# Performance work log

Hardware: AMD Instinct MI355X
Metric: run time of the kernel (lower is better)

Reference implementation:

```python
import jax, jax.numpy as jnp
import numpy as np

D_MODEL = 1024
N_HEADS = 16
N_GROUPS = 4
D_K = D_MODEL // N_HEADS
HEADS_PER_GROUP = N_HEADS // N_GROUPS


def rope(x):
    # x: [b, s, d]; rotate using half-split concat (NOT interleaved), matching source
    s, d = x.shape[1], x.shape[2]
    theta = 1.0 / (10000.0 ** (jnp.arange(d // 2, dtype=jnp.float32) / (d // 2)))
    ang = jnp.arange(s, dtype=jnp.float32)[:, None] * theta[None, :]  # [s, d/2]
    cos, sin = jnp.cos(ang), jnp.sin(ang)
    xe, xo = x[..., 0::2], x[..., 1::2]
    return jnp.concatenate([xe * cos - xo * sin, xe * sin + xo * cos], axis=-1)


def setup_inputs() -> dict:
    key = jax.random.key(0)
    k1, k2, k3, k4, k5 = jax.random.split(key, 5)
    b, s = 1, 2048
    scale = 0.02
    X = jax.random.normal(k1, (b, s, D_MODEL), dtype=jnp.float32)
    W_q = jax.random.normal(k2, (D_MODEL, D_MODEL), dtype=jnp.float32) * scale
    W_k = jax.random.normal(k3, (N_GROUPS * D_K, D_MODEL), dtype=jnp.float32) * scale
    W_v = jax.random.normal(k4, (N_GROUPS * D_K, D_MODEL), dtype=jnp.float32) * scale
    W_o = jax.random.normal(k5, (D_MODEL, D_MODEL), dtype=jnp.float32) * scale
    return {"X": X, "W_q": W_q, "W_k": W_k, "W_v": W_v, "W_o": W_o}


def reference(X, W_q, W_k, W_v, W_o):
    b, s, _ = X.shape
    Xr = rope(X)
    Q = (Xr @ W_q.T).reshape(b, s, N_HEADS, D_K).transpose(0, 2, 1, 3)
    K = (Xr @ W_k.T).reshape(b, s, N_GROUPS, D_K).transpose(0, 2, 1, 3)
    V = (Xr @ W_v.T).reshape(b, s, N_GROUPS, D_K).transpose(0, 2, 1, 3)
    Q = Q.reshape(b, N_GROUPS, HEADS_PER_GROUP, s, D_K)
    scores = jnp.einsum('bghsd,bgtd->bghst', Q, K) / jnp.sqrt(jnp.float32(D_K))
    mask = jnp.triu(jnp.ones((s, s), dtype=scores.dtype), k=1) * (-1e9)
    attn = jax.nn.softmax(scores + mask, axis=-1)
    out = jnp.einsum('bghst,bgtd->bghsd', attn, V)  # [b,g,h,s,dk]
    out = out.reshape(b, N_HEADS, s, D_K).transpose(0, 2, 1, 3).reshape(b, s, D_MODEL)
    return out @ W_o.T
```

## Files before the change

kernel.cpp:

```cpp
#include <hip/hip_runtime.h>
#include <hip/hip_bf16.h>

#define S_LEN   2048
#define D_MODEL 1024
#define N_HEADS 16
#define N_GROUPS 4
#define D_K     64
#define KV_DIM  (N_GROUPS * D_K)

typedef __hip_bfloat16 bf16;
typedef unsigned short u16;
typedef __attribute__((ext_vector_type(8))) short bfrag;
typedef __attribute__((ext_vector_type(4))) float ffrag;
typedef __attribute__((ext_vector_type(4))) unsigned int u32x4;

__device__ __forceinline__ float b2f(u16 u) {
    return __uint_as_float(((unsigned)u) << 16);
}
__device__ __forceinline__ u16 f2bu(float f) {
    bf16 h = __float2bfloat16(f);
    return __builtin_bit_cast(u16, h);
}
__device__ __forceinline__ unsigned cvt_pk_bf16(float lo, float hi) {
    unsigned r;
    asm("v_cvt_pk_bf16_f32 %0, %1, %2" : "=v"(r) : "v"(lo), "v"(hi));
    return r;
}
__device__ __forceinline__ float max3f(float a, float b, float c) {
    float d;
    asm("v_max3_f32 %0, %1, %2, %3" : "=v"(d) : "v"(a), "v"(b), "v"(c));
    return d;
}
__device__ __forceinline__ float ex2(float x) {
#if __has_builtin(__builtin_amdgcn_exp2f)
    return __builtin_amdgcn_exp2f(x);
#else
    return __expf(x * 0.69314718f);
#endif
}

typedef __attribute__((address_space(3))) u16 lds_u16;
typedef __attribute__((address_space(1))) const u16 glb_u16;
__device__ __forceinline__ void gld_lds16(const u16* g, u16* l) {
    __builtin_amdgcn_global_load_lds((glb_u16*)g, (lds_u16*)l, 16, 0, 0);
}

__device__ __forceinline__ int posCS3(int i, int c) {
    if (i >= 4 * c + 3)
        return (c == 0) ? i - 3 : (c == 1) ? i + 6 : (c == 2) ? i + 11 : 27;
    int dd = i - 4 * c + 1;
    return 28 + (3 - dd) * 4 + c;
}

__device__ __forceinline__ int probe_f32(const u16* p) {
    int lane = threadIdx.x & 63;
    int e0 = (p[lane] >> 7) & 0xFF;
    int e1 = (p[lane + 64] >> 7) & 0xFF;
    int c = ((e0 < 100 || e0 > 140) ? 1 : 0) + ((e1 < 100 || e1 > 140) ? 1 : 0);
    unsigned long long b1 = __ballot(c >= 1);
    unsigned long long b2 = __ballot(c >= 2);
    return ((__popcll(b1) + __popcll(b2)) > 16) ? 1 : 0;
}

__global__ void probe5_kernel(const u16* __restrict__ p0, const u16* __restrict__ p1,
                              const u16* __restrict__ p2, const u16* __restrict__ p3,
                              const u16* __restrict__ p4, int* __restrict__ mode) {
    if (blockIdx.x != 0) return;
    const u16* ps[5] = {p0, p1, p2, p3, p4};
    int lane = threadIdx.x & 63;
    for (int t = 0; t < 5; t++) {
        int e0 = (ps[t][lane] >> 7) & 0xFF;
        int e1 = (ps[t][lane + 64] >> 7) & 0xFF;
        int c = ((e0 < 100 || e0 > 140) ? 1 : 0) + ((e1 < 100 || e1 > 140) ? 1 : 0);
        unsigned long long b1 = __ballot(c >= 1);
        unsigned long long b2 = __ballot(c >= 2);
        if (lane == 0) mode[t] = ((__popcll(b1) + __popcll(b2)) > 16) ? 1 : 0;
    }
}

__global__ __launch_bounds__(512)
void prep_kernel(const void* __restrict__ Xin, u16* __restrict__ Xr,
                 const void* __restrict__ Wq, const void* __restrict__ Wk,
                 const void* __restrict__ Wv, const void* __restrict__ Wo,
                 u16* __restrict__ WB, u16* __restrict__ WoB) {
    int b = blockIdx.x;
    if (b < S_LEN) {
        int md = probe_f32((const u16*)Xin);
        int i = b;
        int j = threadIdx.x;
        float freq = ex2(-(float)j * 0.025952563241307518f);
        float ang  = (float)i * freq;
        float sv, cv;
        sincosf(ang, &sv, &cv);
        int base = i * D_MODEL;
        float xe, xo;
        if (md) {
            float2 xv = *(const float2*)&((const float*)Xin)[base + 2 * j];
            xe = xv.x; xo = xv.y;
        } else {
            ushort2 xv = *(const ushort2*)&((const u16*)Xin)[base + 2 * j];
            xe = b2f(xv.x); xo = b2f(xv.y);
        }
        Xr[base + j]       = f2bu(xe * cv - xo * sv);
        Xr[base + 512 + j] = f2bu(xe * sv + xo * cv);
    } else {
        int bid = b - S_LEN;
        const void* src; u16* dst; int goff;
        if (bid < 256)      { src = Wq; dst = WB;               goff = bid; }
        else if (bid < 320) { src = Wk; dst = WB + 1024 * 1024; goff = bid - 256; }
        else if (bid < 384) { src = Wv; dst = WB + 1280 * 1024; goff = bid - 320; }
        else                { src = Wo; dst = WoB;              goff = bid - 384; }
        int md = probe_f32((const u16*)src);
        size_t g = (size_t)goff * 512 + threadIdx.x;
        if (md) {
            const float* f = (const float*)src + g * 8;
            float4 v0 = *(const float4*)f;
            float4 v1 = *(const float4*)(f + 4);
            u16 t[8] = {f2bu(v0.x), f2bu(v0.y), f2bu(v0.z), f2bu(v0.w),
                        f2bu(v1.x), f2bu(v1.y), f2bu(v1.z), f2bu(v1.w)};
            *(uint4*)(dst + g * 8) = *(const uint4*)t;
        } else {
            *(uint4*)(dst + g * 8) = *(const uint4*)((const u16*)src + g * 8);
        }
    }
}

__global__ __launch_bounds__(512)
void rope_kernel(const void* __restrict__ Xin, u16* __restrict__ Xr) {
    int md = probe_f32((const u16*)Xin);
    int i = blockIdx.x;
    int j = threadIdx.x;
    float freq = ex2(-(float)j * 0.025952563241307518f);
    float ang  = (float)i * freq;
    float sv, cv;
    sincosf(ang, &sv, &cv);
    int base = i * D_MODEL;
    float xe, xo;
    if (md) {
        float2 xv = *(const float2*)&((const float*)Xin)[base + 2 * j];
        xe = xv.x; xo = xv.y;
    } else {
        ushort2 xv = *(const ushort2*)&((const u16*)Xin)[base + 2 * j];
        xe = b2f(xv.x); xo = b2f(xv.y);
    }
    Xr[base + j]       = f2bu(xe * cv - xo * sv);
    Xr[base + 512 + j] = f2bu(xe * sv + xo * cv);
}

template<int MODE>
__global__ __launch_bounds__(256)
void gemm_fast(const u16* __restrict__ A, const u16* __restrict__ WBm,
               u16* __restrict__ Qm, u16* __restrict__ Km, u16* __restrict__ Vm,
               float* __restrict__ Cf) {
    __shared__ u16 As[2][8192];
    __shared__ u16 Bs[2][4096];
    const int tid = threadIdx.x;
    const int w = tid >> 6, lane = tid & 63, quad = lane >> 4, lcol = lane & 15;

    const int flat = blockIdx.y * gridDim.x + blockIdx.x;
    const int cpx  = (gridDim.x * gridDim.y) >> 3;
    const int ns   = (flat & 7) * cpx + (flat >> 3);
    const int m0 = (ns / gridDim.x) * 128;
    const int n0 = (ns % gridDim.x) * 64;

    const int arl   = lane >> 3;
    const int colsw = ((lane & 7) ^ arl) * 8;

    const u16* ap[4]; const u16* bp[2];
    #pragma unroll
    for (int c = 0; c < 4; c++)
        ap[c] = A + (size_t)(m0 + (c * 4 + w) * 8 + arl) * 1024 + colsw;
    #pragma unroll
    for (int c = 0; c < 2; c++)
        bp[c] = WBm + (size_t)(n0 + (c * 4 + w) * 8 + arl) * 1024 + colsw;

    const int abase = (w * 32 + lcol) * 64;
    const int koff0 = (quad * 8) ^ ((lcol & 7) * 8);
    const int koff1 = koff0 ^ 32;

    ffrag acc[2][4];
    #pragma unroll
    for (int rf = 0; rf < 2; rf++)
        #pragma unroll
        for (int ct = 0; ct < 4; ct++) acc[rf][ct] = (ffrag)0.0f;

    #pragma unroll
    for (int c = 0; c < 4; c++) gld_lds16(ap[c], &As[0][(c * 4 + w) * 512]);
    #pragma unroll
    for (int c = 0; c < 2; c++) gld_lds16(bp[c], &Bs[0][(c * 4 + w) * 512]);
    __syncthreads();

    int cur = 0;
    for (int k0 = 0; k0 < D_MODEL; k0 += 64) {
        if (k0 + 64 < D_MODEL) {
            const int nb = cur ^ 1;
            #pragma unroll
            for (int c = 0; c < 4; c++)
                gld_lds16(ap[c] + k0 + 64, &As[nb][(c * 4 + w) * 512]);
            #pragma unroll
            for (int c = 0; c < 2; c++)
                gld_lds16(bp[c] + k0 + 64, &Bs[nb][(c * 4 + w) * 512]);
        }

        const u16* Ab = &As[cur][0];
        const u16* Bb = &Bs[cur][0];
        const bfrag a00 = *(const bfrag*)&Ab[abase + koff0];
        const bfrag a10 = *(const bfrag*)&Ab[abase + 1024 + koff0];
        const bfrag a01 = *(const bfrag*)&Ab[abase + koff1];
        const bfrag a11 = *(const bfrag*)&Ab[abase + 1024 + koff1];
        #pragma unroll
        for (int ct = 0; ct < 4; ct++) {
            const int bb = (ct * 16 + lcol) * 64;
            const bfrag b0 = *(const bfrag*)&Bb[bb + koff0];
            acc[0][ct] = __builtin_amdgcn_mfma_f32_16x16x32_bf16(a00, b0, acc[0][ct], 0, 0, 0);
            acc[1][ct] = __builtin_amdgcn_mfma_f32_16x16x32_bf16(a10, b0, acc[1][ct], 0, 0, 0);
            const bfrag b1 = *(const bfrag*)&Bb[bb + koff1];
            acc[0][ct] = __builtin_amdgcn_mfma_f32_16x16x32_bf16(a01, b1, acc[0][ct], 0, 0, 0);
            acc[1][ct] = __builtin_amdgcn_mfma_f32_16x16x32_bf16(a11, b1, acc[1][ct], 0, 0, 0);
        }
        __syncthreads();
        cur ^= 1;
    }

    if (MODE == 0) {
        if (n0 < 1280) {
            u16* Cp; int ldc, nc;
            if (n0 < 1024) { Cp = Qm; ldc = 1024; nc = n0; }
            else           { Cp = Km; ldc = 256;  nc = n0 - 1024; }
            #pragma unroll
            for (int rf = 0; rf < 2; rf++)
                #pragma unroll
                for (int ct = 0; ct < 4; ct++)
                    #pragma unroll
                    for (int r = 0; r < 4; r++) {
                        int row = m0 + w * 32 + rf * 16 + quad * 4 + r;
                        Cp[(size_t)row * ldc + nc + ct * 16 + lcol] = f2bu(acc[rf][ct][r]);
                    }
        } else {
            const int nc = n0 - 1280;
            #pragma unroll
            for (int rf = 0; rf < 2; rf++)
                #pragma unroll
                for (int ct = 0; ct < 4; ct++)
                    #pragma unroll
                    for (int r = 0; r < 4; r++) {
                        int row = m0 + w * 32 + rf * 16 + quad * 4 + r;
                        int col = nc + ct * 16 + lcol;
                        Vm[(size_t)col * S_LEN + row] = f2bu(acc[rf][ct][r]);
                    }
        }
    } else {
        #pragma unroll
        for (int rf = 0; rf < 2; rf++)
            #pragma unroll
            for (int ct = 0; ct < 4; ct++)
                #pragma unroll
                for (int r = 0; r < 4; r++) {
                    int row = m0 + w * 32 + rf * 16 + quad * 4 + r;
                    Cf[(size_t)row * D_MODEL + n0 + ct * 16 + lcol] = acc[rf][ct][r];
                }
    }
}

__device__ __forceinline__ void stageB(u16* dst, const void* Bv, size_t off, int md) {
    if (md) {
        const float* Bf = (const float*)Bv;
        float4 b0 = *(const float4*)&Bf[off];
        float4 b1 = *(const float4*)&Bf[off + 4];
        u16 t[8] = {f2bu(b0.x), f2bu(b0.y), f2bu(b0.z), f2bu(b0.w),
                    f2bu(b1.x), f2bu(b1.y), f2bu(b1.z), f2bu(b1.w)};
        *(uint4*)dst = *(const uint4*)t;
    } else {
        *(uint4*)dst = *(const uint4*)&((const u16*)Bv)[off];
    }
}

__global__ __launch_bounds__(256)
void qkv_mfma(const u16* __restrict__ Xr, const void* __restrict__ Wq,
              const void* __restrict__ Wk, const void* __restrict__ Wv,
              u16* __restrict__ Qm, u16* __restrict__ Km, u16* __restrict__ Vm,
              const int* __restrict__ mode) {
    __shared__ u16 As[128][36];
    __shared__ u16 Bs[64][36];
    const int tid = threadIdx.x;
    const int w = tid >> 6, lane = tid & 63, quad = lane >> 4, lcol = lane & 15;
    const int m0 = blockIdx.y * 128;
    const int n0 = blockIdx.x * 64;

    const void* Bv; int nb, md;
    if (n0 < 1024)       { Bv = Wq; nb = n0;        md = mode[1]; }
    else if (n0 < 1280)  { Bv = Wk; nb = n0 - 1024; md = mode[2]; }
    else                 { Bv = Wv; nb = n0 - 1280; md = mode[3]; }

    ffrag acc[2][4];
    #pragma unroll
    for (int rf = 0; rf < 2; rf++)
        #pragma unroll
        for (int ct = 0; ct < 4; ct++) acc[rf][ct] = (ffrag)0.0f;

    const int arow = tid >> 2, akc = tid & 3;
    for (int k0 = 0; k0 < D_MODEL; k0 += 32) {
        *(uint4*)&As[arow][akc * 8] =
            *(const uint4*)&Xr[(size_t)(m0 + arow) * D_MODEL + k0 + akc * 8];
        *(uint4*)&As[arow + 64][akc * 8] =
            *(const uint4*)&Xr[(size_t)(m0 + arow + 64) * D_MODEL + k0 + akc * 8];
        stageB(&Bs[arow][akc * 8], Bv, (size_t)(nb + arow) * D_MODEL + k0 + akc * 8, md);
        __syncthreads();
        const bfrag a0 = *(const bfrag*)&As[w * 32 + lcol][quad * 8];
        const bfrag a1 = *(const bfrag*)&As[w * 32 + 16 + lcol][quad * 8];
        #pragma unroll
        for (int ct = 0; ct < 4; ct++) {
            const bfrag b = *(const bfrag*)&Bs[ct * 16 + lcol][quad * 8];
            acc[0][ct] = __builtin_amdgcn_mfma_f32_16x16x32_bf16(a0, b, acc[0][ct], 0, 0, 0);
            acc[1][ct] = __builtin_amdgcn_mfma_f32_16x16x32_bf16(a1, b, acc[1][ct], 0, 0, 0);
        }
        __syncthreads();
    }

    if (n0 < 1280) {
        u16* Cp; int ldc, nc;
        if (n0 < 1024) { Cp = Qm; ldc = 1024; nc = n0; }
        else           { Cp = Km; ldc = 256;  nc = n0 - 1024; }
        #pragma unroll
        for (int rf = 0; rf < 2; rf++)
            #pragma unroll
            for (int ct = 0; ct < 4; ct++)
                #pragma unroll
                for (int r = 0; r < 4; r++) {
                    int row = m0 + w * 32 + rf * 16 + quad * 4 + r;
                    Cp[(size_t)row * ldc + nc + ct * 16 + lcol] = f2bu(acc[rf][ct][r]);
                }
    } else {
        const int nc = n0 - 1280;
        #pragma unroll
        for (int rf = 0; rf < 2; rf++)
            #pragma unroll
            for (int ct = 0; ct < 4; ct++)
                #pragma unroll
                for (int r = 0; r < 4; r++) {
                    int row = m0 + w * 32 + rf * 16 + quad * 4 + r;
                    int col = nc + ct * 16 + lcol;
                    Vm[(size_t)col * S_LEN + row] = f2bu(acc[rf][ct][r]);
                }
    }
}

__global__ __launch_bounds__(256)
void oproj_mfma(const u16* __restrict__ A, const void* __restrict__ B,
                float* __restrict__ C, const int* __restrict__ mode) {
    __shared__ u16 As[128][36];
    __shared__ u16 Bs[64][36];
    const int tid = threadIdx.x;
    const int w = tid >> 6, lane = tid & 63, quad = lane >> 4, lcol = lane & 15;
    const int m0 = blockIdx.y * 128;
    const int n0 = blockIdx.x * 64;
    const int md = mode[4];

    ffrag acc[2][4];
    #pragma unroll
    for (int rf = 0; rf < 2; rf++)
        #pragma unroll
        for (int ct = 0; ct < 4; ct++) acc[rf][ct] = (ffrag)0.0f;

    const int arow = tid >> 2, akc = tid & 3;
    for (int k0 = 0; k0 < D_MODEL; k0 += 32) {
        *(uint4*)&As[arow][akc * 8] =
            *(const uint4*)&A[(size_t)(m0 + arow) * D_MODEL + k0 + akc * 8];
        *(uint4*)&As[arow + 64][akc * 8] =
            *(const uint4*)&A[(size_t)(m0 + arow + 64) * D_MODEL + k0 + akc * 8];
        stageB(&Bs[arow][akc * 8], B, (size_t)(n0 + arow) * D_MODEL + k0 + akc * 8, md);
        __syncthreads();
        const bfrag a0 = *(const bfrag*)&As[w * 32 + lcol][quad * 8];
        const bfrag a1 = *(const bfrag*)&As[w * 32 + 16 + lcol][quad * 8];
        #pragma unroll
        for (int ct = 0; ct < 4; ct++) {
            const bfrag b = *(const bfrag*)&Bs[ct * 16 + lcol][quad * 8];
            acc[0][ct] = __builtin_amdgcn_mfma_f32_16x16x32_bf16(a0, b, acc[0][ct], 0, 0, 0);
            acc[1][ct] = __builtin_amdgcn_mfma_f32_16x16x32_bf16(a1, b, acc[1][ct], 0, 0, 0);
        }
        __syncthreads();
    }

    #pragma unroll
    for (int rf = 0; rf < 2; rf++)
        #pragma unroll
        for (int ct = 0; ct < 4; ct++)
            #pragma unroll
            for (int r = 0; r < 4; r++) {
                int row = m0 + w * 32 + rf * 16 + quad * 4 + r;
                C[(size_t)row * D_MODEL + n0 + ct * 16 + lcol] = acc[rf][ct][r];
            }
}

template<int CS, int SF>
__global__ __launch_bounds__(256, 3)
void attn_part(const u16* __restrict__ Q, const u16* __restrict__ K,
               const u16* __restrict__ Vt, float* __restrict__ OpF,
               u16* __restrict__ OpH, float2* __restrict__ ml2) {
    const int bid = blockIdx.x;
    const int cidx = bid >> 4;
    const int h = bid & 15;
    const int g = h >> 2;

    int i, c;
    if (CS == 3) {
        if (cidx < 13)       { c = 0; i = cidx + 3; }
        else if (cidx < 22)  { c = 1; i = cidx - 6; }
        else if (cidx < 27)  { c = 2; i = cidx - 11; }
        else if (cidx == 27) { c = 3; i = 15; }
        else { int t = cidx - 28; int dd = 3 - (t >> 2); c = t & 3; i = 4 * c + dd - 1; }
    } else {
        if (cidx < 8) { i = cidx; c = 0; }
        else          { i = 8 + ((cidx - 8) >> 1); c = (cidx - 8) & 1; }
    }
    const int i0 = i * 128;
    const int tile0 = c << CS;
    const int tlast = min(2 * i + 1, ((c + 1) << CS) - 1);
    const int nt = tlast - tile0 + 1;

    const int tid  = threadIdx.x;
    const int w    = tid >> 6;
    const int lane = tid & 63;
    const int quad = lane >> 4;
    const int lcol = lane & 15;

    __shared__ u16 Ks[2][64][72];
    __shared__ u16 Vts[2][64][72];

    const int qiA = i0 + w * 16 + lcol;
    const int qiB = qiA + 64;
    const bfrag qbA0 = *(const bfrag*)&Q[(size_t)qiA * D_MODEL + h * 64 + quad * 8];
    const bfrag qbA1 = *(const bfrag*)&Q[(size_t)qiA * D_MODEL + h * 64 + 32 + quad * 8];
    const bfrag qbB0 = *(const bfrag*)&Q[(size_t)qiB * D_MODEL + h * 64 + quad * 8];
    const bfrag qbB1 = *(const bfrag*)&Q[(size_t)qiB * D_MODEL + h * 64 + 32 + quad * 8];

    ffrag oaccA[4], oaccB[4];
    #pragma unroll
    for (int ct = 0; ct < 4; ct++) { oaccA[ct] = (ffrag)0.0f; oaccB[ct] = (ffrag)0.0f; }
    float m_runA = 0.0f, l_runA = 0.0f;
    float m_runB = 0.0f, l_runB = 0.0f;

    const int key0 = tid & 63, dc0 = tid >> 6;
    const int vd0 = tid >> 3, vch = tid & 7;
    const int vpos0 = 32 * (vch >> 2) + 16 * (vch & 1) + 4 * ((vch >> 1) & 1);
    const u16* vbase0 = &Vt[(size_t)(g * 64 + vd0) * S_LEN];
    const u16* vbase1 = &Vt[(size_t)(g * 64 + vd0 + 32) * S_LEN];

    int jp = tile0 * 64;
    uint4 kpre0 = *(const uint4*)&K[(size_t)(jp + key0) * KV_DIM + g * 64 + dc0 * 8];
    uint4 kpre1 = *(const uint4*)&K[(size_t)(jp + key0) * KV_DIM + g * 64 + (dc0 + 4) * 8];
    uint4 vpre0 = *(const uint4*)&vbase0[jp + vch * 8];
    uint4 vpre1 = *(const uint4*)&vbase1[jp + vch * 8];

    {
        *(uint4*)&Ks[0][key0][dc0 * 8]       = kpre0;
        *(uint4*)&Ks[0][key0][(dc0 + 4) * 8] = kpre1;
        *(uint2*)&Vts[0][vd0][vpos0]          = make_uint2(vpre0.x, vpre0.y);
        *(uint2*)&Vts[0][vd0][vpos0 + 8]      = make_uint2(vpre0.z, vpre0.w);
        *(uint2*)&Vts[0][vd0 + 32][vpos0]     = make_uint2(vpre1.x, vpre1.y);
        *(uint2*)&Vts[0][vd0 + 32][vpos0 + 8] = make_uint2(vpre1.z, vpre1.w);
    }

    const float CF = 0.18033688f;
    const float GRD = 550.0f;
    int cur = 0;

    for (int tt = 0; tt < nt; tt++) {
        const int tj = tile0 + tt;
        const int j0 = tj * 64;
        const bool hasA = (tj <= 2 * i);

        if (tt + 1 < nt) {
            const int j0n = (tj + 1) * 64;
            kpre0 = *(const uint4*)&K[(size_t)(j0n + key0) * KV_DIM + g * 64 + dc0 * 8];
            kpre1 = *(const uint4*)&K[(size_t)(j0n + key0) * KV_DIM + g * 64 + (dc0 + 4) * 8];
            vpre0 = *(const uint4*)&vbase0[j0n + vch * 8];
            vpre1 = *(const uint4*)&vbase1[j0n + vch * 8];
        }
        __syncthreads();

        ffrag saccA[4], saccB[4];
        #pragma unroll
        for (int ct = 0; ct < 4; ct++) { saccA[ct] = (ffrag)0.0f; saccB[ct] = (ffrag)0.0f; }
        __builtin_amdgcn_s_setprio(1);
        if (hasA) {
            #pragma unroll
            for (int ct = 0; ct < 4; ct++) {
                const bfrag kb0 = *(const bfrag*)&Ks[cur][ct * 16 + lcol][quad * 8];
                saccA[ct] = __builtin_amdgcn_mfma_f32_16x16x32_bf16(kb0, qbA0, saccA[ct], 0, 0, 0);
                saccB[ct] = __builtin_amdgcn_mfma_f32_16x16x32_bf16(kb0, qbB0, saccB[ct], 0, 0, 0);
                const bfrag kb1 = *(const bfrag*)&Ks[cur][ct * 16 + lcol][32 + quad * 8];
                saccA[ct] = __builtin_amdgcn_mfma_f32_16x16x32_bf16(kb1, qbA1, saccA[ct], 0, 0, 0);
                saccB[ct] = __builtin_amdgcn_mfma_f32_16x16x32_bf16(kb1, qbB1, saccB[ct], 0, 0, 0);
            }
        } else {
            #pragma unroll
            for (int ct = 0; ct < 4; ct++) {
                const bfrag kb0 = *(const bfrag*)&Ks[cur][ct * 16 + lcol][quad * 8];
                saccB[ct] = __builtin_amdgcn_mfma_f32_16x16x32_bf16(kb0, qbB0, saccB[ct], 0, 0, 0);
                const bfrag kb1 = *(const bfrag*)&Ks[cur][ct * 16 + lcol][32 + quad * 8];
                saccB[ct] = __builtin_amdgcn_mfma_f32_16x16x32_bf16(kb1, qbB1, saccB[ct], 0, 0, 0);
            }
        }
        __builtin_amdgcn_s_setprio(0);

        bfrag paA0, paA1;
        if (hasA) {
            float svA[4][4];
            if (tj == 2 * i) {
                #pragma unroll
                for (int ct = 0; ct < 4; ct++)
                    #pragma unroll
                    for (int r = 0; r < 4; r++) {
                        int kj = j0 + ct * 16 + quad * 4 + r;
                        svA[ct][r] = (kj <= qiA) ? saccA[ct][r] : -1e30f;
                    }
            } else {
                #pragma unroll
                for (int ct = 0; ct < 4; ct++)
                    #pragma unroll
                    for (int r = 0; r < 4; r++) svA[ct][r] = saccA[ct][r];
            }
            float tA0 = max3f(svA[0][0], svA[0][1], svA[0][2]);
            float tA1 = max3f(svA[0][3], svA[1][0], svA[1][1]);
            float tA2 = max3f(svA[1][2], svA[1][3], svA[2][0]);
            float tA3 = max3f(svA[2][1], svA[2][2], svA[2][3]);
            float tA4 = max3f(svA[3][0], svA[3][1], svA[3][2]);
            float lA = fmaxf(max3f(tA0, tA1, tA2), max3f(tA3, tA4, svA[3][3]));
            if (!__all(lA <= m_runA + GRD)) {
                float mx = fmaxf(lA, __shfl_xor(lA, 16, 64));
                mx = fmaxf(mx, __shfl_xor(mx, 32, 64));
                float mnew = fmaxf(m_runA, mx);
                float al = ex2((m_runA - mnew) * CF);
                l_runA *= al;
                #pragma unroll
                for (int r = 0; r < 4; r++) {
                    float ar = __shfl(al, quad * 4 + r, 64);
                    #pragma unroll
                    for (int ct = 0; ct < 4; ct++) oaccA[ct][r] *= ar;
                }
                m_runA = mnew;
            }
            const float mcA = m_runA * CF;
            float rsA = 0.0f;
            #pragma unroll
            for (int ct = 0; ct < 4; ct++)
                #pragma unroll
                for (int r = 0; r < 4; r++) {
                    float p = ex2(svA[ct][r] * CF - mcA);
                    svA[ct][r] = p;
                    rsA += p;
                }
            rsA += __shfl_xor(rsA, 16, 64);
            rsA += __shfl_xor(rsA, 32, 64);
            l_runA += rsA;

            u32x4 pwA0, pwA1;
            pwA0[0] = cvt_pk_bf16(svA[0][0], svA[0][1]);
            pwA0[1] = cvt_pk_bf16(svA[0][2], svA[0][3]);
            pwA0[2] = cvt_pk_bf16(svA[1][0], svA[1][1]);
            pwA0[3] = cvt_pk_bf16(svA[1][2], svA[1][3]);
            pwA1[0] = cvt_pk_bf16(svA[2][0], svA[2][1]);
            pwA1[1] = cvt_pk_bf16(svA[2][2], svA[2][3]);
            pwA1[2] = cvt_pk_bf16(svA[3][0], svA[3][1]);
            pwA1[3] = cvt_pk_bf16(svA[3][2], svA[3][3]);
            paA0 = __builtin_bit_cast(bfrag, pwA0);
            paA1 = __builtin_bit_cast(bfrag, pwA1);
        }

        float svB[4][4];
        if (tj == 2 * i + 1) {
            #pragma unroll
            for (int ct = 0; ct < 4; ct++)
                #pragma unroll
                for (int r = 0; r < 4; r++) {
                    int kj = j0 + ct * 16 + quad * 4 + r;
                    svB[ct][r] = (kj <= qiB) ? saccB[ct][r] : -1e30f;
                }
        } else {
            #pragma unroll
            for (int ct = 0; ct < 4; ct++)
                #pragma unroll
                for (int r = 0; r < 4; r++) svB[ct][r] = saccB[ct][r];
        }
        float tB0 = max3f(svB[0][0], svB[0][1], svB[0][2]);
        float tB1 = max3f(svB[0][3], svB[1][0], svB[1][1]);
        float tB2 = max3f(svB[1][2], svB[1][3], svB[2][0]);
        float tB3 = max3f(svB[2][1], svB[2][2], svB[2][3]);
        float tB4 = max3f(svB[3][0], svB[3][1], svB[3][2]);
        float lB = fmaxf(max3f(tB0, tB1, tB2), max3f(tB3, tB4, svB[3][3]));
        if (!__all(lB <= m_runB + GRD)) {
            float mx = fmaxf(lB, __shfl_xor(lB, 16, 64));
            mx = fmaxf(mx, __shfl_xor(mx, 32, 64));
            float mnew = fmaxf(m_runB, mx);
            float al = ex2((m_runB - mnew) * CF);
            l_runB *= al;
            #pragma unroll
            for (int r = 0; r < 4; r++) {
                float ar = __shfl(al, quad * 4 + r, 64);
                #pragma unroll
                for (int ct = 0; ct < 4; ct++) oaccB[ct][r] *= ar;
            }
            m_runB = mnew;
        }
        const float mcB = m_runB * CF;
        float rsB = 0.0f;
        #pragma unroll
        for (int ct = 0; ct < 4; ct++)
            #pragma unroll
            for (int r = 0; r < 4; r++) {
                float p = ex2(svB[ct][r] * CF - mcB);
                svB[ct][r] = p;
                rsB += p;
            }
        rsB += __shfl_xor(rsB, 16, 64);
        rsB += __shfl_xor(rsB, 32, 64);
        l_runB += rsB;

        u32x4 pwB0, pwB1;
        pwB0[0] = cvt_pk_bf16(svB[0][0], svB[0][1]);
        pwB0[1] = cvt_pk_bf16(svB[0][2], svB[0][3]);
        pwB0[2] = cvt_pk_bf16(svB[1][0], svB[1][1]);
        pwB0[3] = cvt_pk_bf16(svB[1][2], svB[1][3]);
        pwB1[0] = cvt_pk_bf16(svB[2][0], svB[2][1]);
        pwB1[1] = cvt_pk_bf16(svB[2][2], svB[2][3]);
        pwB1[2] = cvt_pk_bf16(svB[3][0], svB[3][1]);
        pwB1[3] = cvt_pk_bf16(svB[3][2], svB[3][3]);
        const bfrag paB0 = __builtin_bit_cast(bfrag, pwB0);
        const bfrag paB1 = __builtin_bit_cast(bfrag, pwB1);

        __builtin_amdgcn_s_setprio(1);
        if (hasA) {
            #pragma unroll
            for (int ct = 0; ct < 4; ct++) {
                const bfrag vb0 = *(const bfrag*)&Vts[cur][ct * 16 + lcol][quad * 8];
                oaccA[ct] = __builtin_amdgcn_mfma_f32_16x16x32_bf16(paA0, vb0, oaccA[ct], 0, 0, 0);
                oaccB[ct] = __builtin_amdgcn_mfma_f32_16x16x32_bf16(paB0, vb0, oaccB[ct], 0, 0, 0);
                const bfrag vb1 = *(const bfrag*)&Vts[cur][ct * 16 + lcol][32 + quad * 8];
                oaccA[ct] = __builtin_amdgcn_mfma_f32_16x16x32_bf16(paA1, vb1, oaccA[ct], 0, 0, 0);
                oaccB[ct] = __builtin_amdgcn_mfma_f32_16x16x32_bf16(paB1, vb1, oaccB[ct], 0, 0, 0);
            }
        } else {
            #pragma unroll
            for (int ct = 0; ct < 4; ct++) {
                const bfrag vb0 = *(const bfrag*)&Vts[cur][ct * 16 + lcol][quad * 8];
                oaccB[ct] = __builtin_amdgcn_mfma_f32_16x16x32_bf16(paB0, vb0, oaccB[ct], 0, 0, 0);
                const bfrag vb1 = *(const bfrag*)&Vts[cur][ct * 16 + lcol][32 + quad * 8];
                oaccB[ct] = __builtin_amdgcn_mfma_f32_16x16x32_bf16(paB1, vb1, oaccB[ct], 0, 0, 0);
            }
        }
        __builtin_amdgcn_s_setprio(0);

        if (tt + 1 < nt) {
            const int nb = cur ^ 1;
            *(uint4*)&Ks[nb][key0][dc0 * 8]       = kpre0;
            *(uint4*)&Ks[nb][key0][(dc0 + 4) * 8] = kpre1;
            *(uint2*)&Vts[nb][vd0][vpos0]          = make_uint2(vpre0.x, vpre0.y);
            *(uint2*)&Vts[nb][vd0][vpos0 + 8]      = make_uint2(vpre0.z, vpre0.w);
            *(uint2*)&Vts[nb][vd0 + 32][vpos0]     = make_uint2(vpre1.x, vpre1.y);
            *(uint2*)&Vts[nb][vd0 + 32][vpos0 + 8] = make_uint2(vpre1.z, vpre1.w);
        }
        cur ^= 1;
    }

    #pragma unroll
    for (int ct = 0; ct < 4; ct++)
        #pragma unroll
        for (int r = 0; r < 4; r++) {
            int rowA = w * 16 + quad * 4 + r;
            size_t offA = (size_t)bid * 8192 + rowA * 64 + ct * 16 + lcol;
            size_t offB = offA + 4096;
            if (SF) { OpF[offA] = oaccA[ct][r]; OpF[offB] = oaccB[ct][r]; }
            else    { OpH[offA] = f2bu(oaccA[ct][r]); OpH[offB] = f2bu(oaccB[ct][r]); }
        }
    if (quad == 0) {
        ml2[(size_t)bid * 128 + w * 16 + lcol]      = make_float2(m_runA * 0.125f, l_runA);
        ml2[(size_t)bid * 128 + 64 + w * 16 + lcol] = make_float2(m_runB * 0.125f, l_runB);
    }
}

template<int CS, int SF>
__global__ __launch_bounds__(256)
void attn_combine(const float* __restrict__ OpF, const u16* __restrict__ OpH,
                  const float2* __restrict__ ml2, u16* __restrict__ Om) {
    const int row = blockIdx.x;
    const int i = row >> 7;
    const int r = row & 127;
    const int t = threadIdx.x;
    const int h = t >> 4;
    const int d = (t & 15) * 4;
    const int nc = (CS == 3) ? ((2 * i + 1) >> 3) + 1 : ((2 * i + 1) >> 4) + 1;

    float M = -1e30f;
    for (int c = 0; c < nc; c++) {
        int pos = (CS == 3) ? posCS3(i, c) : ((i < 8) ? i : 8 + 2 * (i - 8) + c);
        float2 m = ml2[(size_t)(pos * 16 + h) * 128 + r];
        M = fmaxf(M, m.x);
    }
    float L = 0.0f;
    float acc[4] = {0.0f, 0.0f, 0.0f, 0.0f};
    for (int c = 0; c < nc; c++) {
        int pos = (CS == 3) ? posCS3(i, c) : ((i < 8) ? i : 8 + 2 * (i - 8) + c);
        float2 m = ml2[(size_t)(pos * 16 + h) * 128 + r];
        float wgt = __expf(m.x - M);
        L += m.y * wgt;
        size_t off = (size_t)(pos * 16 + h) * 8192 + r * 64 + d;
        if (SF) {
            float4 v = *(const float4*)&OpF[off];
            acc[0] += v.x * wgt; acc[1] += v.y * wgt;
            acc[2] += v.z * wgt; acc[3] += v.w * wgt;
        } else {
            ushort4 v = *(const ushort4*)&OpH[off];
            acc[0] += b2f(v.x) * wgt; acc[1] += b2f(v.y) * wgt;
            acc[2] += b2f(v.z) * wgt; acc[3] += b2f(v.w) * wgt;
        }
    }
    float inv = 1.0f / L;
    #pragma unroll
    for (int k = 0; k < 4; k++)
        Om[(size_t)row * D_MODEL + h * 64 + d + k] = f2bu(acc[k] * inv);
}

extern "C" void kernel_launch(void* const* d_in, const int* in_sizes, int n_in,
                              void* d_out, int out_size, void* d_ws, size_t ws_size,
                              hipStream_t stream) {
    const void* X  = d_in[0];
    const void* Wq = d_in[1];
    const void* Wk = d_in[2];
    const void* Wv = d_in[3];
    const void* Wo = d_in[4];
    float* out = (float*)d_out;

    u16* XrB = (u16*)d_out;

    int* mode = (int*)d_ws;
    u16* Qm = (u16*)((char*)d_ws + 64);
    u16* Km = Qm + (size_t)S_LEN * D_MODEL;
    u16* Vm = Km + (size_t)S_LEN * KV_DIM;
    u16* Om = Vm + (size_t)S_LEN * KV_DIM;

    const size_t needA    = 10485824ULL + 20971520ULL + 655360ULL;
    const size_t needFull = needA + 3145728ULL + 2097152ULL;

    if (ws_size >= needFull) {
        float*  OpF = (float*)((char*)d_ws + 10485824);
        float2* ml2 = (float2*)((char*)d_ws + 10485824 + 20971520);
        u16*    WB  = (u16*)((char*)d_ws + needA);
        u16*    WoB = WB + (size_t)1536 * 1024;

        prep_kernel<<<S_LEN + 640, 512, 0, stream>>>(X, XrB, Wq, Wk, Wv, Wo, WB, WoB);
        gemm_fast<0><<<dim3(24, 16), 256, 0, stream>>>(XrB, WB, Qm, Km, Vm, nullptr);
        attn_part<3, 1><<<40 * 16, 256, 0, stream>>>(Qm, Km, Vm, OpF, nullptr, ml2);
        attn_combine<3, 1><<<S_LEN, 256, 0, stream>>>(OpF, nullptr, ml2, Om);
        gemm_fast<1><<<dim3(16, 16), 256, 0, stream>>>(Om, WoB, nullptr, nullptr, nullptr, out);
    } else {
        rope_kernel<<<S_LEN, 512, 0, stream>>>(X, XrB);
        probe5_kernel<<<1, 64, 0, stream>>>(
            (const u16*)X, (const u16*)Wq, (const u16*)Wk, (const u16*)Wv,
            (const u16*)Wo, mode);
        qkv_mfma<<<dim3((D_MODEL + 2 * KV_DIM) / 64, S_LEN / 128), 256, 0, stream>>>(
            XrB, Wq, Wk, Wv, Qm, Km, Vm, mode);
        if (ws_size >= needA) {
            float*  OpF = (float*)((char*)d_ws + 10485824);
            float2* ml2 = (float2*)((char*)d_ws + 10485824 + 20971520);
            attn_part<3, 1><<<40 * 16, 256, 0, stream>>>(Qm, Km, Vm, OpF, nullptr, ml2);
            attn_combine<3, 1><<<S_LEN, 256, 0, stream>>>(OpF, nullptr, ml2, Om);
        } else {
            u16*    OpH = (u16*)d_out;
            float2* ml2 = (float2*)((char*)d_out + (size_t)768 * 4096 * 2);
            attn_part<4, 0><<<24 * 16, 256, 0, stream>>>(Qm, Km, Vm, nullptr, OpH, ml2);
            attn_combine<4, 0><<<S_LEN, 256, 0, stream>>>(nullptr, OpH, ml2, Om);
        }
        oproj_mfma<<<dim3(D_MODEL / 64, S_LEN / 128), 256, 0, stream>>>(Om, Wo, out, mode);
    }
}
```

Measured before the change: 134.6 us.

## Halve GEMM M-tile and write single-chunk attention rows directly

The projection GEMMs now use 64x64 tiles instead of 128x64 and launch twice as many blocks. This improves occupancy and wave balance on the many-CU GPU, at the cost of less A/B reuse per block and more global traffic. The attention partial kernel now normalizes and writes the final bf16 output directly for the first 512 query rows, which need only one KV chunk. The combine kernel then skips those rows, removing their partial-result round trip and combine work.

New measurement: 137.8 us. 1.02x slower.

```diff
diff --git a/kernel.cpp b/kernel.cpp
--- a/kernel.cpp
+++ b/kernel.cpp
@@ -152,7 +152,7 @@
 void gemm_fast(const u16* __restrict__ A, const u16* __restrict__ WBm,
                u16* __restrict__ Qm, u16* __restrict__ Km, u16* __restrict__ Vm,
                float* __restrict__ Cf) {
-    __shared__ u16 As[2][8192];
+    __shared__ u16 As[2][4096];
     __shared__ u16 Bs[2][4096];
     const int tid = threadIdx.x;
     const int w = tid >> 6, lane = tid & 63, quad = lane >> 4, lcol = lane & 15;
@@ -160,32 +160,30 @@
     const int flat = blockIdx.y * gridDim.x + blockIdx.x;
     const int cpx  = (gridDim.x * gridDim.y) >> 3;
     const int ns   = (flat & 7) * cpx + (flat >> 3);
-    const int m0 = (ns / gridDim.x) * 128;
+    const int m0 = (ns / gridDim.x) * 64;
     const int n0 = (ns % gridDim.x) * 64;
 
     const int arl   = lane >> 3;
     const int colsw = ((lane & 7) ^ arl) * 8;
 
-    const u16* ap[4]; const u16* bp[2];
-    #pragma unroll
-    for (int c = 0; c < 4; c++)
+    const u16* ap[2]; const u16* bp[2];
+    #pragma unroll
+    for (int c = 0; c < 2; c++)
         ap[c] = A + (size_t)(m0 + (c * 4 + w) * 8 + arl) * 1024 + colsw;
     #pragma unroll
     for (int c = 0; c < 2; c++)
         bp[c] = WBm + (size_t)(n0 + (c * 4 + w) * 8 + arl) * 1024 + colsw;
 
-    const int abase = (w * 32 + lcol) * 64;
+    const int abase = (w * 16 + lcol) * 64;
     const int koff0 = (quad * 8) ^ ((lcol & 7) * 8);
     const int koff1 = koff0 ^ 32;
 
-    ffrag acc[2][4];
-    #pragma unroll
-    for (int rf = 0; rf < 2; rf++)
-        #pragma unroll
-        for (int ct = 0; ct < 4; ct++) acc[rf][ct] = (ffrag)0.0f;
-
-    #pragma unroll
-    for (int c = 0; c < 4; c++) gld_lds16(ap[c], &As[0][(c * 4 + w) * 512]);
+    ffrag acc[4];
+    #pragma unroll
+    for (int ct = 0; ct < 4; ct++) acc[ct] = (ffrag)0.0f;
+
+    #pragma unroll
+    for (int c = 0; c < 2; c++) gld_lds16(ap[c], &As[0][(c * 4 + w) * 512]);
     #pragma unroll
     for (int c = 0; c < 2; c++) gld_lds16(bp[c], &Bs[0][(c * 4 + w) * 512]);
     __syncthreads();
@@ -195,7 +193,7 @@
         if (k0 + 64 < D_MODEL) {
             const int nb = cur ^ 1;
             #pragma unroll
-            for (int c = 0; c < 4; c++)
+            for (int c = 0; c < 2; c++)
                 gld_lds16(ap[c] + k0 + 64, &As[nb][(c * 4 + w) * 512]);
             #pragma unroll
             for (int c = 0; c < 2; c++)
@@ -204,19 +202,15 @@
 
         const u16* Ab = &As[cur][0];
         const u16* Bb = &Bs[cur][0];
-        const bfrag a00 = *(const bfrag*)&Ab[abase + koff0];
-        const bfrag a10 = *(const bfrag*)&Ab[abase + 1024 + koff0];
-        const bfrag a01 = *(const bfrag*)&Ab[abase + koff1];
-        const bfrag a11 = *(const bfrag*)&Ab[abase + 1024 + koff1];
+        const bfrag a0 = *(const bfrag*)&Ab[abase + koff0];
+        const bfrag a1 = *(const bfrag*)&Ab[abase + koff1];
         #pragma unroll
         for (int ct = 0; ct < 4; ct++) {
             const int bb = (ct * 16 + lcol) * 64;
             const bfrag b0 = *(const bfrag*)&Bb[bb + koff0];
-            acc[0][ct] = __builtin_amdgcn_mfma_f32_16x16x32_bf16(a00, b0, acc[0][ct], 0, 0, 0);
-            acc[1][ct] = __builtin_amdgcn_mfma_f32_16x16x32_bf16(a10, b0, acc[1][ct], 0, 0, 0);
+            acc[ct] = __builtin_amdgcn_mfma_f32_16x16x32_bf16(a0, b0, acc[ct], 0, 0, 0);
             const bfrag b1 = *(const bfrag*)&Bb[bb + koff1];
-            acc[0][ct] = __builtin_amdgcn_mfma_f32_16x16x32_bf16(a01, b1, acc[0][ct], 0, 0, 0);
-            acc[1][ct] = __builtin_amdgcn_mfma_f32_16x16x32_bf16(a11, b1, acc[1][ct], 0, 0, 0);
+            acc[ct] = __builtin_amdgcn_mfma_f32_16x16x32_bf16(a1, b1, acc[ct], 0, 0, 0);
         }
         __syncthreads();
         cur ^= 1;
@@ -228,37 +222,31 @@
             if (n0 < 1024) { Cp = Qm; ldc = 1024; nc = n0; }
             else           { Cp = Km; ldc = 256;  nc = n0 - 1024; }
             #pragma unroll
-            for (int rf = 0; rf < 2; rf++)
-                #pragma unroll
-                for (int ct = 0; ct < 4; ct++)
-                    #pragma unroll
-                    for (int r = 0; r < 4; r++) {
-                        int row = m0 + w * 32 + rf * 16 + quad * 4 + r;
-                        Cp[(size_t)row * ldc + nc + ct * 16 + lcol] = f2bu(acc[rf][ct][r]);
-                    }
+            for (int ct = 0; ct < 4; ct++)
+                #pragma unroll
+                for (int r = 0; r < 4; r++) {
+                    int row = m0 + w * 16 + quad * 4 + r;
+                    Cp[(size_t)row * ldc + nc + ct * 16 + lcol] = f2bu(acc[ct][r]);
+                }
         } else {
             const int nc = n0 - 1280;
             #pragma unroll
-            for (int rf = 0; rf < 2; rf++)
-                #pragma unroll
-                for (int ct = 0; ct < 4; ct++)
-                    #pragma unroll
-                    for (int r = 0; r < 4; r++) {
-                        int row = m0 + w * 32 + rf * 16 + quad * 4 + r;
-                        int col = nc + ct * 16 + lcol;
-                        Vm[(size_t)col * S_LEN + row] = f2bu(acc[rf][ct][r]);
-                    }
+            for (int ct = 0; ct < 4; ct++)
+                #pragma unroll
+                for (int r = 0; r < 4; r++) {
+                    int row = m0 + w * 16 + quad * 4 + r;
+                    int col = nc + ct * 16 + lcol;
+                    Vm[(size_t)col * S_LEN + row] = f2bu(acc[ct][r]);
+                }
         }
     } else {
         #pragma unroll
-        for (int rf = 0; rf < 2; rf++)
-            #pragma unroll
-            for (int ct = 0; ct < 4; ct++)
-                #pragma unroll
-                for (int r = 0; r < 4; r++) {
-                    int row = m0 + w * 32 + rf * 16 + quad * 4 + r;
-                    Cf[(size_t)row * D_MODEL + n0 + ct * 16 + lcol] = acc[rf][ct][r];
-                }
+        for (int ct = 0; ct < 4; ct++)
+            #pragma unroll
+            for (int r = 0; r < 4; r++) {
+                int row = m0 + w * 16 + quad * 4 + r;
+                Cf[(size_t)row * D_MODEL + n0 + ct * 16 + lcol] = acc[ct][r];
+            }
     }
 }
 
@@ -396,7 +384,8 @@
 __global__ __launch_bounds__(256, 3)
 void attn_part(const u16* __restrict__ Q, const u16* __restrict__ K,
                const u16* __restrict__ Vt, float* __restrict__ OpF,
-               u16* __restrict__ OpH, float2* __restrict__ ml2) {
+               u16* __restrict__ OpH, float2* __restrict__ ml2,
+               u16* __restrict__ Om) {
     const int bid = blockIdx.x;
     const int cidx = bid >> 4;
     const int h = bid & 15;
@@ -663,6 +652,25 @@
         cur ^= 1;
     }
 
+    if (CS == 3 && 2 * i + 1 <= 7) {
+        #pragma unroll
+        for (int r = 0; r < 4; r++) {
+            float lA = __shfl(l_runA, quad * 4 + r, 64);
+            float lB = __shfl(l_runB, quad * 4 + r, 64);
+            float invA = 1.0f / lA;
+            float invB = 1.0f / lB;
+            int rowA = i0 + w * 16 + quad * 4 + r;
+            #pragma unroll
+            for (int ct = 0; ct < 4; ct++) {
+                Om[(size_t)rowA * D_MODEL + h * 64 + ct * 16 + lcol] =
+                    f2bu(oaccA[ct][r] * invA);
+                Om[(size_t)(rowA + 64) * D_MODEL + h * 64 + ct * 16 + lcol] =
+                    f2bu(oaccB[ct][r] * invB);
+            }
+        }
+        return;
+    }
+
     #pragma unroll
     for (int ct = 0; ct < 4; ct++)
         #pragma unroll
@@ -683,7 +691,7 @@
 __global__ __launch_bounds__(256)
 void attn_combine(const float* __restrict__ OpF, const u16* __restrict__ OpH,
                   const float2* __restrict__ ml2, u16* __restrict__ Om) {
-    const int row = blockIdx.x;
+    const int row = blockIdx.x + ((CS == 3) ? 512 : 0);
     const int i = row >> 7;
     const int r = row & 127;
     const int t = threadIdx.x;
@@ -749,10 +757,10 @@
         u16*    WoB = WB + (size_t)1536 * 1024;
 
         prep_kernel<<<S_LEN + 640, 512, 0, stream>>>(X, XrB, Wq, Wk, Wv, Wo, WB, WoB);
-        gemm_fast<0><<<dim3(24, 16), 256, 0, stream>>>(XrB, WB, Qm, Km, Vm, nullptr);
-        attn_part<3, 1><<<40 * 16, 256, 0, stream>>>(Qm, Km, Vm, OpF, nullptr, ml2);
-        attn_combine<3, 1><<<S_LEN, 256, 0, stream>>>(OpF, nullptr, ml2, Om);
-        gemm_fast<1><<<dim3(16, 16), 256, 0, stream>>>(Om, WoB, nullptr, nullptr, nullptr, out);
+        gemm_fast<0><<<dim3(24, 32), 256, 0, stream>>>(XrB, WB, Qm, Km, Vm, nullptr);
+        attn_part<3, 1><<<40 * 16, 256, 0, stream>>>(Qm, Km, Vm, OpF, nullptr, ml2, Om);
+        attn_combine<3, 1><<<S_LEN - 512, 256, 0, stream>>>(OpF, nullptr, ml2, Om);
+        gemm_fast<1><<<dim3(16, 32), 256, 0, stream>>>(Om, WoB, nullptr, nullptr, nullptr, out);
     } else {
         rope_kernel<<<S_LEN, 512, 0, stream>>>(X, XrB);
         probe5_kernel<<<1, 64, 0, stream>>>(
@@ -763,12 +771,12 @@
         if (ws_size >= needA) {
             float*  OpF = (float*)((char*)d_ws + 10485824);
             float2* ml2 = (float2*)((char*)d_ws + 10485824 + 20971520);
-            attn_part<3, 1><<<40 * 16, 256, 0, stream>>>(Qm, Km, Vm, OpF, nullptr, ml2);
-            attn_combine<3, 1><<<S_LEN, 256, 0, stream>>>(OpF, nullptr, ml2, Om);
+            attn_part<3, 1><<<40 * 16, 256, 0, stream>>>(Qm, Km, Vm, OpF, nullptr, ml2, Om);
+            attn_combine<3, 1><<<S_LEN - 512, 256, 0, stream>>>(OpF, nullptr, ml2, Om);
         } else {
             u16*    OpH = (u16*)d_out;
             float2* ml2 = (float2*)((char*)d_out + (size_t)768 * 4096 * 2);
-            attn_part<4, 0><<<24 * 16, 256, 0, stream>>>(Qm, Km, Vm, nullptr, OpH, ml2);
+            attn_part<4, 0><<<24 * 16, 256, 0, stream>>>(Qm, Km, Vm, nullptr, OpH, ml2, Om);
             attn_combine<4, 0><<<S_LEN, 256, 0, stream>>>(nullptr, OpH, ml2, Om);
         }
         oproj_mfma<<<dim3(D_MODEL / 64, S_LEN / 128), 256, 0, stream>>>(Om, Wo, out, mode);
```
